# Kernel tuning notes

Hardware: AMD Instinct MI355X
Metric: run time of the kernel (lower is better)

Reference implementation:

```python
import jax, jax.numpy as jnp
import numpy as np

OUT_F, IN_F = 4096, 4096
N_FREQ = 10000
SCALING = 150.0


def iwht(x):
    """Unnormalized fast Walsh-Hadamard transform along axis 0. x: [n, m], n power of 2."""
    n, m = x.shape
    steps = int(np.log2(n))
    x = x.reshape((2,) * steps + (m,))
    for ax in range(steps):  # log2(n) butterfly stages
        a, b = jnp.split(x, 2, axis=ax)
        x = jnp.concatenate([a + b, a - b], axis=ax)
    return x.reshape(n, m)


def setup_inputs() -> dict:
    key = jax.random.key(0)
    k1, k2, k3, k4 = jax.random.split(key, 4)
    x = jax.random.normal(k1, (2, 512, IN_F), dtype=jnp.float32)
    weight = jax.random.normal(k2, (OUT_F, IN_F), dtype=jnp.float32) * 0.02
    spectrum = jax.random.normal(k3, (N_FREQ,), dtype=jnp.float32)
    indices = jax.random.randint(k4, (2, N_FREQ), 0, OUT_F, dtype=jnp.int64)
    return {"x": x, "weight": weight, "spectrum": spectrum, "indices": indices}


def reference(x, weight, spectrum, indices):
    out_f, in_f = weight.shape
    # sparse scatter of spectrum into dense (out, in) matrix
    dense = jnp.zeros((out_f, in_f), dtype=spectrum.dtype).at[indices[0], indices[1]].set(spectrum)
    # inverse WHT along out axis, scaled
    delta_w = iwht(dense) * (SCALING / np.sqrt(np.float32(out_f)))
    # F.linear(x, base_w + delta_w)
    return jnp.einsum('bsi,oi->bso', x, weight + delta_w.astype(x.dtype))
```

## Files before the change

### kernel.cpp

```cpp
#include <hip/hip_runtime.h>

typedef unsigned short ushort_t;

#define M_DIM 1024
#define N_DIM 4096
#define K_DIM 4096
#define NFREQ 10000
constexpr float SCALE = 150.0f / 64.0f;

typedef __bf16 bf16x8_t __attribute__((ext_vector_type(8)));
typedef float  f32x4_t  __attribute__((ext_vector_type(4)));

__device__ inline ushort_t f2bf(float f) {
  union { float f; unsigned u; } v; v.f = f;
  unsigned r = v.u + 0x7fffu + ((v.u >> 16) & 1u);
  return (ushort_t)(r >> 16);
}

__global__ __launch_bounds__(256) void build_w4(
    const float* __restrict__ weight,
    const float* __restrict__ spectrum,
    const int* __restrict__ idx,
    const float* __restrict__ x,
    ushort_t* __restrict__ wb,
    ushort_t* __restrict__ xb) {
  if (blockIdx.y == 16) {
    int flat = blockIdx.x * 256 + threadIdx.x;
#pragma unroll 4
    for (int k = 0; k < 64; ++k) {
      int i = flat + k * 16384;
      float4 v = ((const float4*)x)[i];
      ushort4 o;
      o.x = f2bf(v.x); o.y = f2bf(v.y); o.z = f2bf(v.z); o.w = f2bf(v.w);
      ((ushort4*)xb)[i] = o;
    }
    return;
  }

  constexpr int CAP = 1024;
  __shared__ unsigned e_raw[CAP];
  __shared__ float    v_raw[CAP];
  __shared__ uint2    ev_srt[CAP];
  __shared__ int cnt;
  __shared__ int cstart[65];
  __shared__ int coff[64];
  __shared__ int ccnt[64];
  __shared__ unsigned walsh16[16];

  const int tid = threadIdx.x;
  const int ci0 = blockIdx.x * 64;
  const int o0  = blockIdx.y * 256;

  if (tid == 0) cnt = 0;
  if (tid < 64) ccnt[tid] = 0;
  if (tid < 16) {
    unsigned m = tid;
    unsigned w = (m & 1 ? 0xAAAAu : 0u) ^ (m & 2 ? 0xCCCCu : 0u)
               ^ (m & 4 ? 0xF0F0u : 0u) ^ (m & 8 ? 0xFF00u : 0u);
    walsh16[m] = w;
  }
  __syncthreads();

  for (int j = tid; j < NFREQ; j += 256) {
    int c = idx[NFREQ + j];
    if ((c >> 6) == (int)blockIdx.x) {
      int p = atomicAdd(&cnt, 1);
      if (p < CAP) {
        e_raw[p] = ((unsigned)(c & 63) << 26) | ((unsigned)j << 12) | (unsigned)idx[j];
        v_raw[p] = spectrum[j];
        atomicAdd(&ccnt[c & 63], 1);
      }
    }
  }
  __syncthreads();
  const int n = cnt < CAP ? cnt : CAP;

  if (tid < 64) {
    int v = ccnt[tid];
    int s = v;
    for (int d = 1; d < 64; d <<= 1) {
      int o = __shfl_up(s, d, 64);
      if (tid >= d) s += o;
    }
    cstart[tid + 1] = s;
    if (tid == 0) cstart[0] = 0;
    coff[tid] = s - v;
  }
  __syncthreads();
  for (int e = tid; e < n; e += 256) {
    unsigned w = e_raw[e];
    int dc = w >> 26;
    int p = atomicAdd(&coff[dc], 1);
    ev_srt[p] = make_uint2(w, __float_as_uint(v_raw[e]));
  }
  __syncthreads();

  for (int e = tid; e < n; e += 256) {
    uint2 ev = ev_srt[e];
    int dc = ev.x >> 26;
    unsigned r = ev.x & 0xFFFu, j = (ev.x >> 12) & 0x3FFFu;
    int s0 = cstart[dc], e0 = cstart[dc + 1];
    bool dead = false;
    for (int p = s0; p < e0; ++p) {
      unsigned w2 = ev_srt[p].x;
      if ((w2 & 0xFFFu) == r && ((w2 >> 12) & 0x3FFFu) > j) dead = true;
    }
    if (dead) ev_srt[e].y = 0u;
  }
  __syncthreads();

  const int dc0   = (tid & 15) * 4;
  const int rof   = tid >> 4;
  const int obase = o0 + rof * 16;

  float acc[4][16];
#pragma unroll
  for (int c = 0; c < 4; ++c)
#pragma unroll
    for (int j = 0; j < 16; ++j) acc[c][j] = 0.0f;

#pragma unroll
  for (int c = 0; c < 4; ++c) {
    const int s = cstart[dc0 + c], e = cstart[dc0 + c + 1];
    for (int p = s; p < e; ++p) {
      uint2 ev = ev_srt[p];
      unsigned r = ev.x & 0xFFFu;
      unsigned W = walsh16[r & 15u];
      unsigned sx = ev.y ^ ((unsigned)(__popc(obase & r) & 1) << 31);
#pragma unroll
      for (int j = 0; j < 16; ++j) {
        acc[c][j] += __uint_as_float(sx ^ ((W << (31 - j)) & 0x80000000u));
      }
    }
  }

  size_t g = (size_t)obase * K_DIM + ci0 + dc0;
#pragma unroll 4
  for (int j = 0; j < 16; ++j) {
    float4 w4 = *(const float4*)&weight[g];
    ushort4 ov;
    ov.x = f2bf(w4.x + SCALE * acc[0][j]);
    ov.y = f2bf(w4.y + SCALE * acc[1][j]);
    ov.z = f2bf(w4.z + SCALE * acc[2][j]);
    ov.w = f2bf(w4.w + SCALE * acc[3][j]);
    *(ushort4*)&wb[g] = ov;
    g += K_DIM;
  }
}

__global__ __launch_bounds__(256) void gemm_bt(
    const ushort_t* __restrict__ A,
    const ushort_t* __restrict__ B,
    float* __restrict__ C0,
    float* __restrict__ C1,
    int klen) {
  constexpr int BM = 128, BN = 128, BK = 64;
  __shared__ __align__(16) ushort_t As[BM * BK];
  __shared__ __align__(16) ushort_t Bs[BN * BK];

  const int tid  = threadIdx.x;
  const int wave = tid >> 6, lane = tid & 63;
  const int wrow = wave >> 1, wcol = wave & 1;
  const int l16  = lane & 15, quad = lane >> 4;
  const int bm = blockIdx.y * BM, bn = blockIdx.x * BN;
  const int kbeg = blockIdx.z * klen;
  float* __restrict__ dst = blockIdx.z == 0
      ? C0 : C1 + (size_t)(blockIdx.z - 1) * M_DIM * N_DIM;

  const int srow8 = lane >> 3;
  const int sq    = lane & 7;

  f32x4_t acc[4][4] = {};

  for (int kt = kbeg; kt < kbeg + klen; kt += BK) {
#pragma unroll
    for (int c = 0; c < 4; ++c) {
      int ch = wave * 4 + c;
      int gr = ch * 8 + srow8;
      int qg = sq ^ (gr & 7);
      const ushort_t* ga = A + (size_t)(bm + gr) * K_DIM + kt + qg * 8;
      __builtin_amdgcn_global_load_lds(
          (const __attribute__((address_space(1))) void*)ga,
          (__attribute__((address_space(3))) void*)&As[ch * 512], 16, 0, 0);
      const ushort_t* gb = B + (size_t)(bn + gr) * K_DIM + kt + qg * 8;
      __builtin_amdgcn_global_load_lds(
          (const __attribute__((address_space(1))) void*)gb,
          (__attribute__((address_space(3))) void*)&Bs[ch * 512], 16, 0, 0);
    }
    __syncthreads();

    bf16x8_t af[2][4], bfr[2][4];
#pragma unroll
    for (int h = 0; h < 2; ++h) {
#pragma unroll
      for (int i = 0; i < 4; ++i) {
        int kq = h * 4 + quad;
        int ar = wrow * 64 + i * 16 + l16;
        af[h][i]  = *(const bf16x8_t*)&As[ar * BK + ((kq ^ (ar & 7)) * 8)];
        int br = wcol * 64 + i * 16 + l16;
        bfr[h][i] = *(const bf16x8_t*)&Bs[br * BK + ((kq ^ (br & 7)) * 8)];
      }
    }
#pragma unroll
    for (int h = 0; h < 2; ++h)
#pragma unroll
      for (int i = 0; i < 4; ++i)
#pragma unroll
        for (int j = 0; j < 4; ++j)
          acc[i][j] = __builtin_amdgcn_mfma_f32_16x16x32_bf16(af[h][i], bfr[h][j], acc[i][j], 0, 0, 0);
    __syncthreads();
  }

#pragma unroll
  for (int i = 0; i < 4; ++i) {
#pragma unroll
    for (int j = 0; j < 4; ++j) {
      int col = bn + wcol * 64 + j * 16 + l16;
#pragma unroll
      for (int r = 0; r < 4; ++r) {
        int row = bm + wrow * 64 + i * 16 + quad * 4 + r;
        dst[(size_t)row * N_DIM + col] = acc[i][j][r];
      }
    }
  }
}

__global__ __launch_bounds__(256) void reduce_n(float* __restrict__ out,
                                                const float* __restrict__ part,
                                                int npart) {
  int i = blockIdx.x * 256 + threadIdx.x;
  float4 a = ((const float4*)out)[i];
  for (int t = 0; t < npart; ++t) {
    float4 b = ((const float4*)(part + (size_t)t * M_DIM * N_DIM))[i];
    a.x += b.x; a.y += b.y; a.z += b.z; a.w += b.w;
  }
  ((float4*)out)[i] = a;
}

extern "C" void kernel_launch(void* const* d_in, const int* in_sizes, int n_in,
                              void* d_out, int out_size, void* d_ws, size_t ws_size,
                              hipStream_t stream) {
  const float* x        = (const float*)d_in[0];
  const float* weight   = (const float*)d_in[1];
  const float* spectrum = (const float*)d_in[2];
  const int*   indices  = (const int*)d_in[3];
  float* out = (float*)d_out;

  char* ws = (char*)d_ws;
  const size_t WB_BYTES = (size_t)N_DIM * K_DIM * 2;
  const size_t XB_BYTES = (size_t)M_DIM * K_DIM * 2;
  const size_t P1_BYTES = (size_t)M_DIM * N_DIM * 4;

  ushort_t* wb = (ushort_t*)ws;
  ushort_t* xb = (ushort_t*)(ws + WB_BYTES);
  float* part = (float*)(ws + WB_BYTES + XB_BYTES);

  int zsplit;
  if (ws_size >= WB_BYTES + XB_BYTES + 3 * P1_BYTES)      zsplit = 4;
  else if (ws_size >= WB_BYTES + XB_BYTES + P1_BYTES)     zsplit = 2;
  else                                                    zsplit = 1;

  build_w4<<<dim3(64, 17), 256, 0, stream>>>(weight, spectrum, indices, x, wb, xb);

  gemm_bt<<<dim3(N_DIM / 128, M_DIM / 128, zsplit), 256, 0, stream>>>(
      xb, wb, out, part, K_DIM / zsplit);
  if (zsplit > 1)
    reduce_n<<<(M_DIM * N_DIM / 4) / 256, 256, 0, stream>>>(out, part, zsplit - 1);
}
```

Baseline: 226.1 us.

## Apply the sparse Walsh delta to activations instead of densifying it into weights

The sparse spectrum is no longer expanded into a dense 4096x4096 weight update. For each activation row, the spectrum entries are scattered against the matching x values into a 4096-vector in shared memory. An in-LDS fast Walsh-Hadamard transform then produces the row's delta output in fp32, which goes into a partial buffer that the final reduction adds into the GEMM output. The weight bf16 conversion becomes a plain streaming pass, and deduplication of repeated indices moves into a separate small kernel. The trade-offs are an extra 16 MB fp32 partial that must be written and read back, a reduction pass that now always runs, and 1024 LDS-heavy transform blocks.

```diff
diff --git a/kernel.cpp b/kernel.cpp
--- a/kernel.cpp
+++ b/kernel.cpp
@@ -17,18 +17,60 @@
   return (ushort_t)(r >> 16);
 }
 
-__global__ __launch_bounds__(256) void build_w4(
+__global__ __launch_bounds__(256) void dedup(
+    const int* __restrict__ idx,
+    const float* __restrict__ spectrum,
+    unsigned* __restrict__ rc,
+    float* __restrict__ val) {
+  constexpr int CAP = 1024;
+  __shared__ unsigned e_pack[CAP];
+  __shared__ int cnt;
+  const int tid = threadIdx.x;
+
+  if (tid == 0) cnt = 0;
+  __syncthreads();
+  for (int j = tid; j < NFREQ; j += 256) {
+    int c = idx[NFREQ + j];
+    if ((c >> 6) == (int)blockIdx.x) {
+      int p = atomicAdd(&cnt, 1);
+      if (p < CAP)
+        e_pack[p] = ((unsigned)j << 18) | ((unsigned)(c & 63) << 12) | (unsigned)idx[j];
+    }
+  }
+  __syncthreads();
+  const int n = cnt < CAP ? cnt : CAP;
+
+  for (int e = tid; e < n; e += 256) {
+    unsigned w = e_pack[e];
+    unsigned key = w & 0x3FFFFu;
+    unsigned j   = w >> 18;
+    bool dead = false;
+    for (int p = 0; p < n; ++p) {
+      unsigned w2 = e_pack[p];
+      if ((w2 & 0x3FFFFu) == key && (w2 >> 18) > j) dead = true;
+    }
+    int c = (int)((w >> 12) & 63u) + (int)blockIdx.x * 64;
+    rc[j]  = ((w & 0xFFFu) << 12) | (unsigned)c;
+    val[j] = dead ? 0.0f : spectrum[j];
+  }
+}
+
+__global__ __launch_bounds__(256) void fused_pre(
     const float* __restrict__ weight,
-    const float* __restrict__ spectrum,
-    const int* __restrict__ idx,
     const float* __restrict__ x,
+    const unsigned* __restrict__ rc,
+    const float* __restrict__ val,
     ushort_t* __restrict__ wb,
-    ushort_t* __restrict__ xb) {
-  if (blockIdx.y == 16) {
-    int flat = blockIdx.x * 256 + threadIdx.x;
+    ushort_t* __restrict__ xb,
+    float* __restrict__ delta) {
+  const int tid = threadIdx.x;
+  const int bx  = blockIdx.x;
+
+  if (bx >= 3072) {
+    int b3 = bx - 3072;
 #pragma unroll 4
-    for (int k = 0; k < 64; ++k) {
-      int i = flat + k * 16384;
+    for (int k = 0; k < 16; ++k) {
+      int i = b3 * 4096 + k * 256 + tid;
       float4 v = ((const float4*)x)[i];
       ushort4 o;
       o.x = f2bf(v.x); o.y = f2bf(v.y); o.z = f2bf(v.z); o.w = f2bf(v.w);
@@ -36,115 +78,58 @@
     }
     return;
   }
-
-  constexpr int CAP = 1024;
-  __shared__ unsigned e_raw[CAP];
-  __shared__ float    v_raw[CAP];
-  __shared__ uint2    ev_srt[CAP];
-  __shared__ int cnt;
-  __shared__ int cstart[65];
-  __shared__ int coff[64];
-  __shared__ int ccnt[64];
-  __shared__ unsigned walsh16[16];
-
-  const int tid = threadIdx.x;
-  const int ci0 = blockIdx.x * 64;
-  const int o0  = blockIdx.y * 256;
-
-  if (tid == 0) cnt = 0;
-  if (tid < 64) ccnt[tid] = 0;
-  if (tid < 16) {
-    unsigned m = tid;
-    unsigned w = (m & 1 ? 0xAAAAu : 0u) ^ (m & 2 ? 0xCCCCu : 0u)
-               ^ (m & 4 ? 0xF0F0u : 0u) ^ (m & 8 ? 0xFF00u : 0u);
-    walsh16[m] = w;
-  }
-  __syncthreads();
-
-  for (int j = tid; j < NFREQ; j += 256) {
-    int c = idx[NFREQ + j];
-    if ((c >> 6) == (int)blockIdx.x) {
-      int p = atomicAdd(&cnt, 1);
-      if (p < CAP) {
-        e_raw[p] = ((unsigned)(c & 63) << 26) | ((unsigned)j << 12) | (unsigned)idx[j];
-        v_raw[p] = spectrum[j];
-        atomicAdd(&ccnt[c & 63], 1);
-      }
-    }
-  }
-  __syncthreads();
-  const int n = cnt < CAP ? cnt : CAP;
-
-  if (tid < 64) {
-    int v = ccnt[tid];
-    int s = v;
-    for (int d = 1; d < 64; d <<= 1) {
-      int o = __shfl_up(s, d, 64);
-      if (tid >= d) s += o;
-    }
-    cstart[tid + 1] = s;
-    if (tid == 0) cstart[0] = 0;
-    coff[tid] = s - v;
-  }
-  __syncthreads();
-  for (int e = tid; e < n; e += 256) {
-    unsigned w = e_raw[e];
-    int dc = w >> 26;
-    int p = atomicAdd(&coff[dc], 1);
-    ev_srt[p] = make_uint2(w, __float_as_uint(v_raw[e]));
-  }
-  __syncthreads();
-
-  for (int e = tid; e < n; e += 256) {
-    uint2 ev = ev_srt[e];
-    int dc = ev.x >> 26;
-    unsigned r = ev.x & 0xFFFu, j = (ev.x >> 12) & 0x3FFFu;
-    int s0 = cstart[dc], e0 = cstart[dc + 1];
-    bool dead = false;
-    for (int p = s0; p < e0; ++p) {
-      unsigned w2 = ev_srt[p].x;
-      if ((w2 & 0xFFFu) == r && ((w2 >> 12) & 0x3FFFu) > j) dead = true;
-    }
-    if (dead) ev_srt[e].y = 0u;
-  }
-  __syncthreads();
-
-  const int dc0   = (tid & 15) * 4;
-  const int rof   = tid >> 4;
-  const int obase = o0 + rof * 16;
-
-  float acc[4][16];
-#pragma unroll
-  for (int c = 0; c < 4; ++c)
-#pragma unroll
-    for (int j = 0; j < 16; ++j) acc[c][j] = 0.0f;
-
-#pragma unroll
-  for (int c = 0; c < 4; ++c) {
-    const int s = cstart[dc0 + c], e = cstart[dc0 + c + 1];
-    for (int p = s; p < e; ++p) {
-      uint2 ev = ev_srt[p];
-      unsigned r = ev.x & 0xFFFu;
-      unsigned W = walsh16[r & 15u];
-      unsigned sx = ev.y ^ ((unsigned)(__popc(obase & r) & 1) << 31);
-#pragma unroll
-      for (int j = 0; j < 16; ++j) {
-        acc[c][j] += __uint_as_float(sx ^ ((W << (31 - j)) & 0x80000000u));
-      }
-    }
-  }
-
-  size_t g = (size_t)obase * K_DIM + ci0 + dc0;
+  if (bx >= 1024) {
+    int b2 = bx - 1024;
 #pragma unroll 4
-  for (int j = 0; j < 16; ++j) {
-    float4 w4 = *(const float4*)&weight[g];
-    ushort4 ov;
-    ov.x = f2bf(w4.x + SCALE * acc[0][j]);
-    ov.y = f2bf(w4.y + SCALE * acc[1][j]);
-    ov.z = f2bf(w4.z + SCALE * acc[2][j]);
-    ov.w = f2bf(w4.w + SCALE * acc[3][j]);
-    *(ushort4*)&wb[g] = ov;
-    g += K_DIM;
+    for (int k = 0; k < 8; ++k) {
+      int i = b2 * 2048 + k * 256 + tid;
+      float4 v = ((const float4*)weight)[i];
+      ushort4 o;
+      o.x = f2bf(v.x); o.y = f2bf(v.y); o.z = f2bf(v.z); o.w = f2bf(v.w);
+      ((ushort4*)wb)[i] = o;
+    }
+    return;
+  }
+
+  __shared__ float y[N_DIM];
+  const int m = bx;
+  const float* xrow = x + (size_t)m * K_DIM;
+
+  for (int i = tid; i < N_DIM; i += 256) y[i] = 0.0f;
+  __syncthreads();
+
+  for (int t = 0; t < 40; ++t) {
+    int j = t * 256 + tid;
+    if (j < NFREQ) {
+      unsigned p = rc[j];
+      float v = val[j];
+      float xv = xrow[p & 0xFFFu];
+      atomicAdd(&y[p >> 12], v * xv);
+    }
+  }
+  __syncthreads();
+
+  for (int s = 0; s < 12; ++s) {
+    const int stride = 1 << s;
+#pragma unroll
+    for (int b = 0; b < 8; ++b) {
+      int t = b * 256 + tid;
+      int i = ((t >> s) << (s + 1)) | (t & (stride - 1));
+      float lo = y[i], hi = y[i + stride];
+      y[i] = lo + hi;
+      y[i + stride] = lo - hi;
+    }
+    __syncthreads();
+  }
+
+  float* drow = delta + (size_t)m * N_DIM;
+  for (int i = tid; i < N_DIM / 4; i += 256) {
+    float4 o;
+    o.x = SCALE * y[i * 4 + 0];
+    o.y = SCALE * y[i * 4 + 1];
+    o.z = SCALE * y[i * 4 + 2];
+    o.w = SCALE * y[i * 4 + 3];
+    ((float4*)drow)[i] = o;
   }
 }
 
@@ -247,23 +232,28 @@
   float* out = (float*)d_out;
 
   char* ws = (char*)d_ws;
+  const size_t RC_OFF   = 0;
+  const size_t VAL_OFF  = 40960;
+  const size_t WB_OFF   = 81920;
   const size_t WB_BYTES = (size_t)N_DIM * K_DIM * 2;
+  const size_t XB_OFF   = WB_OFF + WB_BYTES;
   const size_t XB_BYTES = (size_t)M_DIM * K_DIM * 2;
+  const size_t PART_OFF = XB_OFF + XB_BYTES;
   const size_t P1_BYTES = (size_t)M_DIM * N_DIM * 4;
 
-  ushort_t* wb = (ushort_t*)ws;
-  ushort_t* xb = (ushort_t*)(ws + WB_BYTES);
-  float* part = (float*)(ws + WB_BYTES + XB_BYTES);
-
-  int zsplit;
-  if (ws_size >= WB_BYTES + XB_BYTES + 3 * P1_BYTES)      zsplit = 4;
-  else if (ws_size >= WB_BYTES + XB_BYTES + P1_BYTES)     zsplit = 2;
-  else                                                    zsplit = 1;
-
-  build_w4<<<dim3(64, 17), 256, 0, stream>>>(weight, spectrum, indices, x, wb, xb);
-
+  unsigned* rc  = (unsigned*)(ws + RC_OFF);
+  float*    val = (float*)(ws + VAL_OFF);
+  ushort_t* wb  = (ushort_t*)(ws + WB_OFF);
+  ushort_t* xb  = (ushort_t*)(ws + XB_OFF);
+  float*    part = (float*)(ws + PART_OFF);
+
+  int navail = ws_size > PART_OFF ? (int)((ws_size - PART_OFF) / P1_BYTES) : 1;
+  int zsplit = navail >= 4 ? 4 : (navail >= 2 ? 2 : 1);
+  float* delta = part + (size_t)(zsplit - 1) * (M_DIM * N_DIM);
+
+  dedup<<<64, 256, 0, stream>>>(indices, spectrum, rc, val);
+  fused_pre<<<3328, 256, 0, stream>>>(weight, x, rc, val, wb, xb, delta);
   gemm_bt<<<dim3(N_DIM / 128, M_DIM / 128, zsplit), 256, 0, stream>>>(
       xb, wb, out, part, K_DIM / zsplit);
-  if (zsplit > 1)
-    reduce_n<<<(M_DIM * N_DIM / 4) / 256, 256, 0, stream>>>(out, part, zsplit - 1);
-}
+  reduce_n<<<(M_DIM * N_DIM / 4) / 256, 256, 0, stream>>>(out, part, zsplit);
+}
```

After: 260.5 us. 1.15x slower.
